# Kernel optimization log

Measured on AMD Instinct MI355X. Metric: run time of the kernel, lower is better.

## Reference

```python
import jax, jax.numpy as jnp
import numpy as np

EMB_DIM = 1024
N_HEADS = 16
HEAD_DIM = EMB_DIM // N_HEADS


def setup_inputs() -> dict:
    key = jax.random.key(0)
    k_x, k_qkv, k_w, k_b = jax.random.split(key, 4)
    x = jax.random.normal(k_x, (2, 2048, EMB_DIM), dtype=jnp.float32)
    # nn.Linear(emb_dim, 3*emb_dim, bias=False): weight [3E, E]; y = x @ W.T
    w_qkv = jax.random.normal(k_qkv, (3 * EMB_DIM, EMB_DIM), dtype=jnp.float32) * (EMB_DIM ** -0.5)
    # nn.Linear(emb_dim, emb_dim) with bias
    w_out = jax.random.normal(k_w, (EMB_DIM, EMB_DIM), dtype=jnp.float32) * (EMB_DIM ** -0.5)
    b_out = jax.random.normal(k_b, (EMB_DIM,), dtype=jnp.float32) * 0.01
    return {"x": x, "w_qkv": w_qkv, "w_out": w_out, "b_out": b_out}


def reference(x, w_qkv, w_out, b_out):
    B, S, E = x.shape
    H, D = N_HEADS, HEAD_DIM
    qkv = jnp.einsum('bse,fe->bsf', x, w_qkv)  # [B,S,3E]
    q, k, v = jnp.split(qkv, 3, axis=-1)
    # [B,S,E] -> [B,H,S,D]
    q = q.reshape(B, S, H, D).transpose(0, 2, 1, 3)
    k = k.reshape(B, S, H, D).transpose(0, 2, 1, 3)
    v = v.reshape(B, S, H, D).transpose(0, 2, 1, 3)
    scale = 1.0 / np.sqrt(D).astype(np.float32)
    scores = jnp.einsum('bhqd,bhkd->bhqk', q, k) * scale  # [B,H,S,S]
    causal = jnp.triu(jnp.ones((S, S), dtype=bool), k=1)
    scores = jnp.where(causal, -jnp.inf, scores)
    probs = jax.nn.softmax(scores, axis=-1)
    attn = jnp.einsum('bhqk,bhkd->bhqd', probs, v)  # [B,H,S,D]
    attn = attn.transpose(0, 2, 1, 3).reshape(B, S, E)
    return jnp.einsum('bse,fe->bsf', attn, w_out) + b_out
```

## Files before the change

kernel.cpp:

```cpp
#include <hip/hip_runtime.h>
#include <hip/hip_bf16.h>

#define EMB 1024
#define NH 16
#define HD 64
#define BATCH 2
#define SEQ 2048
#define MROWS (BATCH*SEQ)
#define F3 (3*EMB)

typedef __bf16 bf16;
typedef __attribute__((ext_vector_type(8))) __bf16 bf16x8;
typedef __attribute__((ext_vector_type(4))) __bf16 bf16x4;
typedef __attribute__((ext_vector_type(2))) __bf16 bf16x2;
typedef __attribute__((ext_vector_type(4))) float f32x4;
typedef __attribute__((ext_vector_type(16))) float f32x16;
typedef __attribute__((ext_vector_type(2))) unsigned int u32x2;

typedef const __attribute__((address_space(1))) void* gptr_t;
typedef __attribute__((address_space(3))) void* lptr_t;
#define GLDS16(g, l) __builtin_amdgcn_global_load_lds((gptr_t)(g), (lptr_t)(l), 16, 0, 0)

__device__ inline bf16 tobf(float f) {
    union { __hip_bfloat16 h; bf16 b; } cv;
    cv.h = __float2bfloat16(f);
    return cv.b;
}

__device__ inline float fexp2(float x) {
#if __has_builtin(__builtin_amdgcn_exp2f)
    return __builtin_amdgcn_exp2f(x);
#else
    return exp2f(x);
#endif
}

__device__ inline void plswap(unsigned& a, unsigned& b) {
#if __has_builtin(__builtin_amdgcn_permlane32_swap)
    u32x2 r = __builtin_amdgcn_permlane32_swap(a, b, false, false);
    a = r[0]; b = r[1];
#else
    unsigned pa = (unsigned)__shfl_xor((int)a, 32, 64);
    unsigned pb = (unsigned)__shfl_xor((int)b, 32, 64);
    bool hi = (threadIdx.x & 32) != 0;
    unsigned na = hi ? pb : a;
    unsigned nb = hi ? b : pa;
    a = na; b = nb;
#endif
}
__device__ inline void plswapf(float& a, float& b) {
    unsigned ua = __builtin_bit_cast(unsigned, a), ub = __builtin_bit_cast(unsigned, b);
    plswap(ua, ub);
    a = __builtin_bit_cast(float, ua); b = __builtin_bit_cast(float, ub);
}
__device__ inline unsigned pack2(float x, float y) {
    bf16x2 t; t[0] = (bf16)x; t[1] = (bf16)y;
    return __builtin_bit_cast(unsigned, t);
}

#define N1 (MROWS*EMB)
#define N2 (F3*EMB)
#define N3 (EMB*EMB)
__global__ __launch_bounds__(256) void cvt_all(const float* __restrict__ x,
                                               const float* __restrict__ wq,
                                               const float* __restrict__ wo,
                                               bf16* __restrict__ xb,
                                               bf16* __restrict__ wqb,
                                               bf16* __restrict__ wob) {
    int i = (blockIdx.x * 256 + threadIdx.x) * 4;
    const float* src;
    bf16* dst;
    int off;
    if (i < N1)           { src = x;  dst = xb;  off = i; }
    else if (i < N1 + N2) { src = wq; dst = wqb; off = i - N1; }
    else                  { src = wo; dst = wob; off = i - N1 - N2; }
    const float4 v = *reinterpret_cast<const float4*>(src + off);
    bf16x4 o;
    o[0] = tobf(v.x); o[1] = tobf(v.y); o[2] = tobf(v.z); o[3] = tobf(v.w);
    *reinterpret_cast<bf16x4*>(dst + off) = o;
}

__global__ __launch_bounds__(256) void gemm_qkv(const bf16* __restrict__ A,
                                                const bf16* __restrict__ Bw,
                                                bf16* __restrict__ qb,
                                                bf16* __restrict__ kb,
                                                bf16* __restrict__ vt) {
    const int K = 1024;
    __shared__ alignas(16) bf16 Alds[128 * 32];
    __shared__ alignas(16) bf16 Blds[128 * 32];
    const int tid = threadIdx.x;
    const int w = tid >> 6, l = tid & 63;
    const int m0 = blockIdx.y * 128, n0 = blockIdx.x * 128;
    const int wr = w >> 1, wc = w & 1;

    f32x4 acc[4][4];
#pragma unroll
    for (int mi = 0; mi < 4; ++mi)
#pragma unroll
        for (int ni = 0; ni < 4; ++ni)
            acc[mi][ni] = f32x4{0.f, 0.f, 0.f, 0.f};

    const int srow = l >> 2;
    const int scol = (l & 3) * 8;
    const bf16* Abase = A + (size_t)m0 * K;
    const bf16* Bbase = Bw + (size_t)n0 * K;

    for (int k0 = 0; k0 < K; k0 += 32) {
#pragma unroll
        for (int i = 0; i < 2; ++i) {
            int chunk = w * 2 + i;
            int row = chunk * 16 + srow;
            GLDS16(Abase + (size_t)row * K + k0 + scol, &Alds[chunk * 512]);
            GLDS16(Bbase + (size_t)row * K + k0 + scol, &Blds[chunk * 512]);
        }
        __syncthreads();
        bf16x8 af[4], bfr[4];
#pragma unroll
        for (int mi = 0; mi < 4; ++mi)
            af[mi] = *reinterpret_cast<const bf16x8*>(
                &Alds[(wr * 64 + mi * 16 + (l & 15)) * 32 + (l >> 4) * 8]);
#pragma unroll
        for (int ni = 0; ni < 4; ++ni)
            bfr[ni] = *reinterpret_cast<const bf16x8*>(
                &Blds[(wc * 64 + ni * 16 + (l & 15)) * 32 + (l >> 4) * 8]);
#pragma unroll
        for (int mi = 0; mi < 4; ++mi)
#pragma unroll
            for (int ni = 0; ni < 4; ++ni)
                acc[mi][ni] = __builtin_amdgcn_mfma_f32_16x16x32_bf16(
                    af[mi], bfr[ni], acc[mi][ni], 0, 0, 0);
        __syncthreads();
    }

    const int which = n0 >> 10;
#pragma unroll
    for (int mi = 0; mi < 4; ++mi) {
#pragma unroll
        for (int ni = 0; ni < 4; ++ni) {
            int fcol = n0 + wc * 64 + ni * 16 + (l & 15);
            int h = (fcol >> 6) & 15, d = fcol & 63;
            int mbase = m0 + wr * 64 + mi * 16 + (l >> 4) * 4;
            int b = mbase >> 11, s = mbase & 2047;
            int bh = b * NH + h;
            if (which == 2) {
                bf16x4 vv;
#pragma unroll
                for (int jj = 0; jj < 4; ++jj) vv[jj] = tobf(acc[mi][ni][jj]);
                *reinterpret_cast<bf16x4*>(&vt[((size_t)bh * HD + d) * SEQ + s]) = vv;
            } else if (which == 0) {
#pragma unroll
                for (int jj = 0; jj < 4; ++jj)
                    qb[((size_t)bh * SEQ + s + jj) * HD + d] = tobf(acc[mi][ni][jj] * 0.180336881f);
            } else {
#pragma unroll
                for (int jj = 0; jj < 4; ++jj)
                    kb[((size_t)bh * SEQ + s + jj) * HD + d] = tobf(acc[mi][ni][jj]);
            }
        }
    }
}

__global__ __launch_bounds__(512, 4) void attn_kernel(const bf16* __restrict__ qb,
                                                      const bf16* __restrict__ kb,
                                                      const bf16* __restrict__ vt,
                                                      bf16* __restrict__ ao) {
    __shared__ alignas(16) char SM[69632];
    bf16 (*Kl)[4096] = (bf16 (*)[4096])SM;
    bf16 (*Vl)[4096] = (bf16 (*)[4096])(SM + 32768);
    float* Msh = (float*)(SM + 65536);
    float* Rsh = (float*)(SM + 67584);
    float* Osh = (float*)SM;

    const int tid = threadIdx.x, w = tid >> 6, l = tid & 63;
    const int hi = l >> 5;
    const int qg = w & 3, kg = w >> 2;
    const int h = (int)(blockIdx.x >> 5);
    const int qt = (h < 8) ? (15 - h) : (h - 8);
    const int bh = blockIdx.x & 31;
    const int q0 = qt * 128;
    const bf16* Qp = qb + (size_t)bh * SEQ * HD;
    const bf16* Kp = kb + (size_t)bh * SEQ * HD;
    const bf16* Vp = vt + (size_t)bh * HD * SEQ;

    const int qa = q0 + qg * 32 + (l & 31);
    bf16x8 qf[4];
#pragma unroll
    for (int kk = 0; kk < 4; ++kk)
        qf[kk] = *reinterpret_cast<const bf16x8*>(&Qp[(size_t)qa * HD + kk * 16 + hi * 8]);

    f32x16 o[2];
#pragma unroll
    for (int t = 0; t < 2; ++t)
#pragma unroll
        for (int r = 0; r < 16; ++r) o[t][r] = 0.f;
    float m = -__builtin_inff(), rs = 0.f;

    const int sc = ((l & 7) ^ (l >> 3)) * 8;

#define STAGE(itp)                                                                  \
    do {                                                                            \
        int j_ = 2 * (itp) + kg;                                                    \
        int slot_ = j_ & 3;                                                         \
        int kv0_ = j_ * 64;                                                         \
        int r0_ = qg * 16 + (l >> 3);                                               \
        GLDS16(Kp + (size_t)(kv0_ + r0_) * HD + sc, &Kl[slot_][(qg * 16) * 64]);    \
        GLDS16(Kp + (size_t)(kv0_ + r0_ + 8) * HD + sc, &Kl[slot_][(qg * 16 + 8) * 64]); \
        GLDS16(Vp + (size_t)r0_ * SEQ + kv0_ + sc, &Vl[slot_][(qg * 16) * 64]);     \
        GLDS16(Vp + (size_t)(r0_ + 8) * SEQ + kv0_ + sc, &Vl[slot_][(qg * 16 + 8) * 64]); \
    } while (0)

    STAGE(0);
    __syncthreads();

    const int qminw = q0 + qg * 32;
    const int qmaxw = qminw + 31;

    for (int it = 0; it <= qt; ++it) {
        if (it < qt) STAGE(it + 1);
        const int j = 2 * it + kg;
        if (j * 64 <= qmaxw) {
            const int slot = j & 3;
            f32x16 st[2];
            __builtin_amdgcn_s_setprio(1);
#pragma unroll
            for (int t = 0; t < 2; ++t) {
#pragma unroll
                for (int r = 0; r < 16; ++r) st[t][r] = 0.f;
                int row = t * 32 + (l & 31);
                int rsw = (row & 7) << 3;
#pragma unroll
                for (int kk = 0; kk < 4; ++kk) {
                    bf16x8 kf = *reinterpret_cast<const bf16x8*>(
                        &Kl[slot][row * 64 + ((kk * 16 + hi * 8) ^ rsw)]);
                    st[t] = __builtin_amdgcn_mfma_f32_32x32x16_bf16(kf, qf[kk], st[t], 0, 0, 0);
                }
            }
            __builtin_amdgcn_s_setprio(0);
            if (j * 64 + 63 > qminw) {
#pragma unroll
                for (int t = 0; t < 2; ++t)
#pragma unroll
                    for (int r = 0; r < 16; ++r) {
                        int kv = j * 64 + t * 32 + 8 * (r >> 2) + 4 * hi + (r & 3);
                        if (kv > qa) st[t][r] = -__builtin_inff();
                    }
            }
            float red[8];
#pragma unroll
            for (int r = 0; r < 8; ++r)
                red[r] = fmaxf(fmaxf(st[0][r], st[0][r + 8]), fmaxf(st[1][r], st[1][r + 8]));
            float pm = fmaxf(fmaxf(fmaxf(red[0], red[1]), fmaxf(red[2], red[3])),
                             fmaxf(fmaxf(red[4], red[5]), fmaxf(red[6], red[7])));
            float pa_ = pm, pb_ = pm;
            plswapf(pa_, pb_);
            pm = fmaxf(pa_, pb_);
            if (!__all(pm <= m + 8.f)) {
                float mn = fmaxf(m, pm);
                float al = fexp2(m - mn);
#pragma unroll
                for (int t = 0; t < 2; ++t)
#pragma unroll
                    for (int r = 0; r < 16; ++r) o[t][r] *= al;
                rs *= al;
                m = mn;
            }
#pragma unroll
            for (int t = 0; t < 2; ++t)
#pragma unroll
                for (int r = 0; r < 16; ++r) {
                    float p = fexp2(st[t][r] - m);
                    st[t][r] = p;
                    rs += p;
                }
#pragma unroll
            for (int t = 0; t < 2; ++t) {
                unsigned Ag[4], Bg[4];
#pragma unroll
                for (int g = 0; g < 4; ++g) {
                    Ag[g] = pack2(st[t][4 * g + 0], st[t][4 * g + 1]);
                    Bg[g] = pack2(st[t][4 * g + 2], st[t][4 * g + 3]);
                }
                __builtin_amdgcn_s_setprio(1);
#pragma unroll
                for (int k2 = 0; k2 < 2; ++k2) {
                    unsigned w0 = Ag[2 * k2], w2 = Ag[2 * k2 + 1];
                    plswap(w0, w2);
                    unsigned w1 = Bg[2 * k2], w3 = Bg[2 * k2 + 1];
                    plswap(w1, w3);
                    union { unsigned u[4]; bf16x8 v; } pf;
                    pf.u[0] = w0; pf.u[1] = w1; pf.u[2] = w2; pf.u[3] = w3;
                    const int kk = 2 * t + k2;
#pragma unroll
                    for (int dt = 0; dt < 2; ++dt) {
                        int row = dt * 32 + (l & 31);
                        bf16x8 vf = *reinterpret_cast<const bf16x8*>(
                            &Vl[slot][row * 64 + ((kk * 16 + hi * 8) ^ ((row & 7) << 3))]);
                        o[dt] = __builtin_amdgcn_mfma_f32_32x32x16_bf16(vf, pf.v, o[dt], 0, 0, 0);
                    }
                }
                __builtin_amdgcn_s_setprio(0);
            }
        }
        __syncthreads();
    }

    float rlo = rs, rhi = rs;
    plswapf(rlo, rhi);
    const float rfull = rlo + rhi;
    Msh[w * 64 + l] = m;
    Rsh[w * 64 + l] = rfull;
    if (kg == 1) {
        float* dst = Osh + (size_t)(qg * 64 + l) * 32;
#pragma unroll
        for (int c = 0; c < 8; ++c) {
            f32x4 tch;
#pragma unroll
            for (int i = 0; i < 4; ++i) tch[i] = o[c >> 2][(c & 3) * 4 + i];
            *reinterpret_cast<f32x4*>(dst + (c ^ (l & 7)) * 4) = tch;
        }
    }
    __syncthreads();
    if (kg == 0) {
        const float mb = Msh[(w + 4) * 64 + l];
        const float rb = Rsh[(w + 4) * 64 + l];
        const float mstar = fmaxf(m, mb);
        const float sa = fexp2(m - mstar), sb = fexp2(mb - mstar);
        const float inv = 1.f / (rfull * sa + rb * sb);
        const float* src = Osh + (size_t)(qg * 64 + l) * 32;
        const int b = bh >> 4, hh = bh & 15;
#pragma unroll
        for (int c = 0; c < 8; ++c) {
            f32x4 ob = *reinterpret_cast<const f32x4*>(src + (c ^ (l & 7)) * 4);
            bf16x4 ov;
#pragma unroll
            for (int i = 0; i < 4; ++i)
                ov[i] = (bf16)((o[c >> 2][(c & 3) * 4 + i] * sa + ob[i] * sb) * inv);
            int d0 = (c >> 2) * 32 + 8 * (c & 3) + 4 * hi;
            *reinterpret_cast<bf16x4*>(&ao[((size_t)b * SEQ + qa) * EMB + hh * HD + d0]) = ov;
        }
    }
#undef STAGE
}

__global__ __launch_bounds__(256) void gemm_out(const bf16* __restrict__ A,
                                                const bf16* __restrict__ Bw,
                                                float* __restrict__ out,
                                                const float* __restrict__ bias) {
    const int K = 1024;
    __shared__ alignas(16) bf16 Alds[64 * 32];
    __shared__ alignas(16) bf16 Blds[128 * 32];
    const int tid = threadIdx.x;
    const int w = tid >> 6, l = tid & 63;
    const int m0 = blockIdx.y * 64, n0 = blockIdx.x * 128;

    f32x4 acc[4][2];
#pragma unroll
    for (int mi = 0; mi < 4; ++mi)
#pragma unroll
        for (int ni = 0; ni < 2; ++ni)
            acc[mi][ni] = f32x4{0.f, 0.f, 0.f, 0.f};

    const int srow = l >> 2;
    const int scol = (l & 3) * 8;
    const bf16* Abase = A + (size_t)m0 * K;
    const bf16* Bbase = Bw + (size_t)n0 * K;

    for (int k0 = 0; k0 < K; k0 += 32) {
        GLDS16(Abase + (size_t)(w * 16 + srow) * K + k0 + scol, &Alds[w * 512]);
#pragma unroll
        for (int i = 0; i < 2; ++i) {
            int chunk = w * 2 + i;
            GLDS16(Bbase + (size_t)(chunk * 16 + srow) * K + k0 + scol, &Blds[chunk * 512]);
        }
        __syncthreads();
        bf16x8 af[4], bfr[2];
#pragma unroll
        for (int mi = 0; mi < 4; ++mi)
            af[mi] = *reinterpret_cast<const bf16x8*>(
                &Alds[(mi * 16 + (l & 15)) * 32 + (l >> 4) * 8]);
#pragma unroll
        for (int ni = 0; ni < 2; ++ni)
            bfr[ni] = *reinterpret_cast<const bf16x8*>(
                &Blds[(w * 32 + ni * 16 + (l & 15)) * 32 + (l >> 4) * 8]);
#pragma unroll
        for (int mi = 0; mi < 4; ++mi)
#pragma unroll
            for (int ni = 0; ni < 2; ++ni)
                acc[mi][ni] = __builtin_amdgcn_mfma_f32_16x16x32_bf16(
                    af[mi], bfr[ni], acc[mi][ni], 0, 0, 0);
        __syncthreads();
    }

#pragma unroll
    for (int mi = 0; mi < 4; ++mi) {
#pragma unroll
        for (int ni = 0; ni < 2; ++ni) {
            int fcol = n0 + w * 32 + ni * 16 + (l & 15);
            float bv = bias[fcol];
#pragma unroll
            for (int jj = 0; jj < 4; ++jj) {
                int m = m0 + mi * 16 + (l >> 4) * 4 + jj;
                out[(size_t)m * EMB + fcol] = acc[mi][ni][jj] + bv;
            }
        }
    }
}

extern "C" void kernel_launch(void* const* d_in, const int* in_sizes, int n_in,
                              void* d_out, int out_size, void* d_ws, size_t ws_size,
                              hipStream_t stream) {
    const float* x     = (const float*)d_in[0];
    const float* w_qkv = (const float*)d_in[1];
    const float* w_out = (const float*)d_in[2];
    const float* b_out = (const float*)d_in[3];
    float* out = (float*)d_out;

    char* ws = (char*)d_ws;
    bf16* xb    = (bf16*)(ws);
    bf16* wqkvb = (bf16*)(ws + ((size_t)8 << 20));
    bf16* woutb = (bf16*)(ws + ((size_t)14 << 20));
    bf16* qb    = (bf16*)(ws + ((size_t)16 << 20));
    bf16* kb    = (bf16*)(ws + ((size_t)24 << 20));
    bf16* vt    = (bf16*)(ws + ((size_t)32 << 20));
    bf16* ab    = (bf16*)(ws + ((size_t)40 << 20));

    cvt_all<<<(N1 + N2 + N3) / 1024, 256, 0, stream>>>(x, w_qkv, w_out, xb, wqkvb, woutb);
    gemm_qkv<<<dim3(F3 / 128, MROWS / 128), 256, 0, stream>>>(xb, wqkvb, qb, kb, vt);
    attn_kernel<<<512, 512, 0, stream>>>(qb, kb, vt, ab);
    gemm_out<<<dim3(EMB / 128, MROWS / 64), 256, 0, stream>>>(ab, woutb, out, b_out);
}
```

Baseline: 170.2 us.

## Rewrite QKV GEMM as 256x256 tile with double-buffered swizzled LDS pipeline

Replaces the simple 128x128 QKV projection GEMM, which synchronised on every K step, with a 256x256 tile per 512-thread block. It uses 128KB of dynamic LDS split into two buffers, XOR-swizzled LDS layout to avoid bank conflicts, and an interleaved schedule that issues global-to-LDS loads for future K tiles while MFMAs run on current fragments. It also adds explicit waitcnt, barriers and setprio to hide load latency and raise data reuse. In exchange it runs far fewer blocks (12x16=192), so occupancy is lower and the CUs may be unevenly loaded, and the hand-written schedule is fragile.

```diff
diff --git a/kernel.cpp b/kernel.cpp
--- a/kernel.cpp
+++ b/kernel.cpp
@@ -80,84 +80,177 @@
     *reinterpret_cast<bf16x4*>(dst + off) = o;
 }
 
-__global__ __launch_bounds__(256) void gemm_qkv(const bf16* __restrict__ A,
-                                                const bf16* __restrict__ Bw,
-                                                bf16* __restrict__ qb,
-                                                bf16* __restrict__ kb,
-                                                bf16* __restrict__ vt) {
-    const int K = 1024;
-    __shared__ alignas(16) bf16 Alds[128 * 32];
-    __shared__ alignas(16) bf16 Blds[128 * 32];
+__global__ __launch_bounds__(512, 2) void gemm_qkv(const bf16* __restrict__ A,
+                                                   const bf16* __restrict__ Bw,
+                                                   bf16* __restrict__ qb,
+                                                   bf16* __restrict__ kb,
+                                                   bf16* __restrict__ vt) {
+    extern __shared__ bf16 dsm[];
+    bf16* Al = dsm;
+    bf16* Bl = dsm + 32768;
+
     const int tid = threadIdx.x;
     const int w = tid >> 6, l = tid & 63;
-    const int m0 = blockIdx.y * 128, n0 = blockIdx.x * 128;
-    const int wr = w >> 1, wc = w & 1;
-
-    f32x4 acc[4][4];
-#pragma unroll
-    for (int mi = 0; mi < 4; ++mi)
-#pragma unroll
-        for (int ni = 0; ni < 4; ++ni)
-            acc[mi][ni] = f32x4{0.f, 0.f, 0.f, 0.f};
-
-    const int srow = l >> 2;
-    const int scol = (l & 3) * 8;
-    const bf16* Abase = A + (size_t)m0 * K;
-    const bf16* Bbase = Bw + (size_t)n0 * K;
-
-    for (int k0 = 0; k0 < K; k0 += 32) {
-#pragma unroll
-        for (int i = 0; i < 2; ++i) {
-            int chunk = w * 2 + i;
-            int row = chunk * 16 + srow;
-            GLDS16(Abase + (size_t)row * K + k0 + scol, &Alds[chunk * 512]);
-            GLDS16(Bbase + (size_t)row * K + k0 + scol, &Blds[chunk * 512]);
-        }
-        __syncthreads();
-        bf16x8 af[4], bfr[4];
-#pragma unroll
-        for (int mi = 0; mi < 4; ++mi)
-            af[mi] = *reinterpret_cast<const bf16x8*>(
-                &Alds[(wr * 64 + mi * 16 + (l & 15)) * 32 + (l >> 4) * 8]);
-#pragma unroll
-        for (int ni = 0; ni < 4; ++ni)
-            bfr[ni] = *reinterpret_cast<const bf16x8*>(
-                &Blds[(wc * 64 + ni * 16 + (l & 15)) * 32 + (l >> 4) * 8]);
-#pragma unroll
-        for (int mi = 0; mi < 4; ++mi)
-#pragma unroll
-            for (int ni = 0; ni < 4; ++ni)
-                acc[mi][ni] = __builtin_amdgcn_mfma_f32_16x16x32_bf16(
-                    af[mi], bfr[ni], acc[mi][ni], 0, 0, 0);
-        __syncthreads();
-    }
-
-    const int which = n0 >> 10;
-#pragma unroll
-    for (int mi = 0; mi < 4; ++mi) {
-#pragma unroll
-        for (int ni = 0; ni < 4; ++ni) {
-            int fcol = n0 + wc * 64 + ni * 16 + (l & 15);
+    const int wm = w >> 2, wn = w & 3;
+    const int m0 = blockIdx.y * 256, n0 = blockIdx.x * 256;
+
+    const int sc = ((l & 7) ^ (l >> 3)) * 8;
+    const int lr = l >> 3;
+    const int l15 = l & 15, l4 = l >> 4, l7 = l & 7;
+
+    f32x4 acc[8][4];
+#pragma unroll
+    for (int i = 0; i < 8; ++i)
+#pragma unroll
+        for (int j = 0; j < 4; ++j) acc[i][j] = f32x4{0.f, 0.f, 0.f, 0.f};
+
+    bf16x8 Af[4][2], Bf[2][2];
+
+#define STA(bb, mh, ct)                                                                  \
+    do {                                                                                 \
+        int rs_ = (mh) * 64 + w * 8;                                                     \
+        GLDS16(A + (size_t)(m0 + rs_ + lr) * 1024 + (ct) * 64 + sc, (lptr_t)&Al[(bb) * 16384 + rs_ * 64]);          \
+        GLDS16(A + (size_t)(m0 + 128 + rs_ + lr) * 1024 + (ct) * 64 + sc, (lptr_t)&Al[(bb) * 16384 + (128 + rs_) * 64]); \
+    } while (0)
+#define STB(bb, nh, ct)                                                                  \
+    do {                                                                                 \
+        int r1_ = (w >> 2) * 64 + (nh) * 32 + (w & 3) * 8;                               \
+        int r2_ = r1_ + 128;                                                             \
+        GLDS16(Bw + (size_t)(n0 + r1_ + lr) * 1024 + (ct) * 64 + sc, (lptr_t)&Bl[(bb) * 16384 + r1_ * 64]); \
+        GLDS16(Bw + (size_t)(n0 + r2_ + lr) * 1024 + (ct) * 64 + sc, (lptr_t)&Bl[(bb) * 16384 + r2_ * 64]); \
+    } while (0)
+#define LDA(bb, mh)                                                                      \
+    do {                                                                                 \
+        _Pragma("unroll") for (int mi = 0; mi < 4; ++mi)                                 \
+        _Pragma("unroll") for (int ks = 0; ks < 2; ++ks)                                 \
+            Af[mi][ks] = *reinterpret_cast<const bf16x8*>(                               \
+                &Al[(bb) * 16384 + (wm * 128 + (mh) * 64 + mi * 16 + l15) * 64 +         \
+                    (((ks * 4 + l4) ^ l7) * 8)]);                                        \
+    } while (0)
+#define LDB(bb, nh)                                                                      \
+    do {                                                                                 \
+        _Pragma("unroll") for (int ni = 0; ni < 2; ++ni)                                 \
+        _Pragma("unroll") for (int ks = 0; ks < 2; ++ks)                                 \
+            Bf[ni][ks] = *reinterpret_cast<const bf16x8*>(                               \
+                &Bl[(bb) * 16384 + (wn * 64 + (nh) * 32 + ni * 16 + l15) * 64 +          \
+                    (((ks * 4 + l4) ^ l7) * 8)]);                                        \
+    } while (0)
+#define MM(mh, nh)                                                                       \
+    do {                                                                                 \
+        __builtin_amdgcn_s_setprio(1);                                                   \
+        _Pragma("unroll") for (int mi = 0; mi < 4; ++mi)                                 \
+        _Pragma("unroll") for (int ni = 0; ni < 2; ++ni)                                 \
+        _Pragma("unroll") for (int ks = 0; ks < 2; ++ks)                                 \
+            acc[(mh) * 4 + mi][(nh) * 2 + ni] = __builtin_amdgcn_mfma_f32_16x16x32_bf16( \
+                Af[mi][ks], Bf[ni][ks], acc[(mh) * 4 + mi][(nh) * 2 + ni], 0, 0, 0);     \
+        __builtin_amdgcn_s_setprio(0);                                                   \
+    } while (0)
+#define PH_TAIL()                                                                        \
+    __builtin_amdgcn_s_barrier();                                                        \
+    asm volatile("s_waitcnt lgkmcnt(0)" ::: "memory");                                   \
+    __builtin_amdgcn_sched_barrier(0)
+#define PH_END() __builtin_amdgcn_s_barrier()
+
+    STA(0, 0, 0); STA(0, 1, 0); STB(0, 0, 0); STB(0, 1, 0);
+    STB(1, 0, 1); STA(1, 1, 1);
+    asm volatile("s_waitcnt vmcnt(4)" ::: "memory");
+    __builtin_amdgcn_s_barrier();
+
+#pragma unroll 1
+    for (int it = 0; it < 7; ++it) {
+        const int t1 = 2 * it + 1;
+        LDA(0, 0); LDB(0, 0);
+        __builtin_amdgcn_sched_barrier(0);
+        STA(1, 0, t1);
+        PH_TAIL(); MM(0, 0); PH_END();
+        LDA(0, 1);
+        __builtin_amdgcn_sched_barrier(0);
+        STB(1, 1, t1);
+        PH_TAIL(); MM(1, 0); PH_END();
+        LDB(0, 1);
+        __builtin_amdgcn_sched_barrier(0);
+        STB(0, 0, t1 + 1);
+        PH_TAIL(); MM(1, 1); PH_END();
+        LDA(0, 0);
+        __builtin_amdgcn_sched_barrier(0);
+        STA(0, 1, t1 + 1);
+        asm volatile("s_waitcnt vmcnt(4)" ::: "memory");
+        PH_TAIL(); MM(0, 1); PH_END();
+        LDA(1, 0); LDB(1, 0);
+        __builtin_amdgcn_sched_barrier(0);
+        STA(0, 0, t1 + 1);
+        PH_TAIL(); MM(0, 0); PH_END();
+        LDA(1, 1);
+        __builtin_amdgcn_sched_barrier(0);
+        STB(0, 1, t1 + 1);
+        PH_TAIL(); MM(1, 0); PH_END();
+        LDB(1, 1);
+        __builtin_amdgcn_sched_barrier(0);
+        STB(1, 0, t1 + 2);
+        PH_TAIL(); MM(1, 1); PH_END();
+        LDA(1, 0);
+        __builtin_amdgcn_sched_barrier(0);
+        STA(1, 1, t1 + 2);
+        asm volatile("s_waitcnt vmcnt(4)" ::: "memory");
+        PH_TAIL(); MM(0, 1); PH_END();
+    }
+    {
+        LDA(0, 0); LDB(0, 0);
+        __builtin_amdgcn_sched_barrier(0);
+        STA(1, 0, 15);
+        PH_TAIL(); MM(0, 0); PH_END();
+        LDA(0, 1);
+        __builtin_amdgcn_sched_barrier(0);
+        STB(1, 1, 15);
+        PH_TAIL(); MM(1, 0); PH_END();
+        LDB(0, 1);
+        PH_TAIL(); MM(1, 1); PH_END();
+        LDA(0, 0);
+        asm volatile("s_waitcnt vmcnt(0)" ::: "memory");
+        PH_TAIL(); MM(0, 1); PH_END();
+        LDA(1, 0); LDB(1, 0);
+        PH_TAIL(); MM(0, 0); PH_END();
+        LDA(1, 1);
+        PH_TAIL(); MM(1, 0); PH_END();
+        LDB(1, 1);
+        PH_TAIL(); MM(1, 1); PH_END();
+        LDA(1, 0);
+        PH_TAIL(); MM(0, 1); PH_END();
+    }
+
+    const int which = (n0 + wn * 64) >> 10;
+#pragma unroll
+    for (int mf = 0; mf < 8; ++mf) {
+#pragma unroll
+        for (int nf = 0; nf < 4; ++nf) {
+            int fcol = n0 + wn * 64 + nf * 16 + l15;
             int h = (fcol >> 6) & 15, d = fcol & 63;
-            int mbase = m0 + wr * 64 + mi * 16 + (l >> 4) * 4;
+            int mbase = m0 + wm * 128 + mf * 16 + l4 * 4;
             int b = mbase >> 11, s = mbase & 2047;
             int bh = b * NH + h;
             if (which == 2) {
                 bf16x4 vv;
 #pragma unroll
-                for (int jj = 0; jj < 4; ++jj) vv[jj] = tobf(acc[mi][ni][jj]);
+                for (int jj = 0; jj < 4; ++jj) vv[jj] = tobf(acc[mf][nf][jj]);
                 *reinterpret_cast<bf16x4*>(&vt[((size_t)bh * HD + d) * SEQ + s]) = vv;
             } else if (which == 0) {
 #pragma unroll
                 for (int jj = 0; jj < 4; ++jj)
-                    qb[((size_t)bh * SEQ + s + jj) * HD + d] = tobf(acc[mi][ni][jj] * 0.180336881f);
+                    qb[((size_t)bh * SEQ + s + jj) * HD + d] = tobf(acc[mf][nf][jj] * 0.180336881f);
             } else {
 #pragma unroll
                 for (int jj = 0; jj < 4; ++jj)
-                    kb[((size_t)bh * SEQ + s + jj) * HD + d] = tobf(acc[mi][ni][jj]);
+                    kb[((size_t)bh * SEQ + s + jj) * HD + d] = tobf(acc[mf][nf][jj]);
             }
         }
     }
+#undef STA
+#undef STB
+#undef LDA
+#undef LDB
+#undef MM
+#undef PH_TAIL
+#undef PH_END
 }
 
 __global__ __launch_bounds__(512, 4) void attn_kernel(const bf16* __restrict__ qb,
@@ -424,8 +517,11 @@
     bf16* vt    = (bf16*)(ws + ((size_t)32 << 20));
     bf16* ab    = (bf16*)(ws + ((size_t)40 << 20));
 
+    hipFuncSetAttribute((const void*)gemm_qkv,
+                        hipFuncAttributeMaxDynamicSharedMemorySize, 131072);
+
     cvt_all<<<(N1 + N2 + N3) / 1024, 256, 0, stream>>>(x, w_qkv, w_out, xb, wqkvb, woutb);
-    gemm_qkv<<<dim3(F3 / 128, MROWS / 128), 256, 0, stream>>>(xb, wqkvb, qb, kb, vt);
+    gemm_qkv<<<dim3(F3 / 256, MROWS / 256), 512, 131072, stream>>>(xb, wqkvb, qb, kb, vt);
     attn_kernel<<<512, 512, 0, stream>>>(qb, kb, vt, ab);
     gemm_out<<<dim3(EMB / 128, MROWS / 64), 256, 0, stream>>>(ab, woutb, out, b_out);
 }
```

Measured after the change: 170.7 us. No clear change (+0.3%).

## Double GEMM K-tile to 64 with XOR-swizzled LDS and block remap

Applied to the files above, without the earlier changes.

Both the QKV and output projection GEMMs now stage 64-wide K tiles instead of 32, halving the number of barrier pairs per K loop. An XOR swizzle is applied to the LDS column placement so the wider rows avoid bank conflicts on the fragment reads. Block indices are also remapped so consecutive workgroups share A/B tiles in L2. Costs are double the LDS footprint per block and more fragment registers, which may reduce occupancy.

```diff
diff --git a/kernel.cpp b/kernel.cpp
--- a/kernel.cpp
+++ b/kernel.cpp
@@ -86,12 +86,18 @@
                                                 bf16* __restrict__ kb,
                                                 bf16* __restrict__ vt) {
     const int K = 1024;
-    __shared__ alignas(16) bf16 Alds[128 * 32];
-    __shared__ alignas(16) bf16 Blds[128 * 32];
+    __shared__ alignas(16) bf16 Alds[128 * 64];
+    __shared__ alignas(16) bf16 Blds[128 * 64];
     const int tid = threadIdx.x;
     const int w = tid >> 6, l = tid & 63;
-    const int m0 = blockIdx.y * 128, n0 = blockIdx.x * 128;
     const int wr = w >> 1, wc = w & 1;
+    const int lin = (int)blockIdx.y * 24 + (int)blockIdx.x;
+    const int swz = (lin & 7) * 96 + (lin >> 3);
+    const int m0 = (swz / 24) * 128, n0 = (swz % 24) * 128;
+
+    const int sc = ((l & 7) ^ (l >> 3)) * 8;
+    const int lr = l >> 3;
+    const int l15 = l & 15, l4 = l >> 4, l7 = l & 7;
 
     f32x4 acc[4][4];
 #pragma unroll
@@ -100,35 +106,38 @@
         for (int ni = 0; ni < 4; ++ni)
             acc[mi][ni] = f32x4{0.f, 0.f, 0.f, 0.f};
 
-    const int srow = l >> 2;
-    const int scol = (l & 3) * 8;
     const bf16* Abase = A + (size_t)m0 * K;
     const bf16* Bbase = Bw + (size_t)n0 * K;
 
-    for (int k0 = 0; k0 < K; k0 += 32) {
-#pragma unroll
-        for (int i = 0; i < 2; ++i) {
-            int chunk = w * 2 + i;
-            int row = chunk * 16 + srow;
-            GLDS16(Abase + (size_t)row * K + k0 + scol, &Alds[chunk * 512]);
-            GLDS16(Bbase + (size_t)row * K + k0 + scol, &Blds[chunk * 512]);
+    for (int k0 = 0; k0 < K; k0 += 64) {
+#pragma unroll
+        for (int i = 0; i < 4; ++i) {
+            int r0 = i * 32 + w * 8;
+            GLDS16(Abase + (size_t)(r0 + lr) * K + k0 + sc, (lptr_t)&Alds[r0 * 64]);
+            GLDS16(Bbase + (size_t)(r0 + lr) * K + k0 + sc, (lptr_t)&Blds[r0 * 64]);
         }
         __syncthreads();
-        bf16x8 af[4], bfr[4];
+        bf16x8 af[4][2], bfr[4][2];
 #pragma unroll
         for (int mi = 0; mi < 4; ++mi)
-            af[mi] = *reinterpret_cast<const bf16x8*>(
-                &Alds[(wr * 64 + mi * 16 + (l & 15)) * 32 + (l >> 4) * 8]);
+#pragma unroll
+            for (int ks = 0; ks < 2; ++ks)
+                af[mi][ks] = *reinterpret_cast<const bf16x8*>(
+                    &Alds[(wr * 64 + mi * 16 + l15) * 64 + (((ks * 4 + l4) ^ l7) * 8)]);
 #pragma unroll
         for (int ni = 0; ni < 4; ++ni)
-            bfr[ni] = *reinterpret_cast<const bf16x8*>(
-                &Blds[(wc * 64 + ni * 16 + (l & 15)) * 32 + (l >> 4) * 8]);
+#pragma unroll
+            for (int ks = 0; ks < 2; ++ks)
+                bfr[ni][ks] = *reinterpret_cast<const bf16x8*>(
+                    &Blds[(wc * 64 + ni * 16 + l15) * 64 + (((ks * 4 + l4) ^ l7) * 8)]);
 #pragma unroll
         for (int mi = 0; mi < 4; ++mi)
 #pragma unroll
             for (int ni = 0; ni < 4; ++ni)
-                acc[mi][ni] = __builtin_amdgcn_mfma_f32_16x16x32_bf16(
-                    af[mi], bfr[ni], acc[mi][ni], 0, 0, 0);
+#pragma unroll
+                for (int ks = 0; ks < 2; ++ks)
+                    acc[mi][ni] = __builtin_amdgcn_mfma_f32_16x16x32_bf16(
+                        af[mi][ks], bfr[ni][ks], acc[mi][ni], 0, 0, 0);
         __syncthreads();
     }
 
@@ -137,9 +146,9 @@
     for (int mi = 0; mi < 4; ++mi) {
 #pragma unroll
         for (int ni = 0; ni < 4; ++ni) {
-            int fcol = n0 + wc * 64 + ni * 16 + (l & 15);
+            int fcol = n0 + wc * 64 + ni * 16 + l15;
             int h = (fcol >> 6) & 15, d = fcol & 63;
-            int mbase = m0 + wr * 64 + mi * 16 + (l >> 4) * 4;
+            int mbase = m0 + wr * 64 + mi * 16 + l4 * 4;
             int b = mbase >> 11, s = mbase & 2047;
             int bh = b * NH + h;
             if (which == 2) {
@@ -347,11 +356,17 @@
                                                 float* __restrict__ out,
                                                 const float* __restrict__ bias) {
     const int K = 1024;
-    __shared__ alignas(16) bf16 Alds[64 * 32];
-    __shared__ alignas(16) bf16 Blds[128 * 32];
+    __shared__ alignas(16) bf16 Alds[64 * 64];
+    __shared__ alignas(16) bf16 Blds[128 * 64];
     const int tid = threadIdx.x;
     const int w = tid >> 6, l = tid & 63;
-    const int m0 = blockIdx.y * 64, n0 = blockIdx.x * 128;
+    const int lin = (int)blockIdx.y * 8 + (int)blockIdx.x;
+    const int swz = (lin & 7) * 64 + (lin >> 3);
+    const int m0 = (swz >> 3) * 64, n0 = (swz & 7) * 128;
+
+    const int sc = ((l & 7) ^ (l >> 3)) * 8;
+    const int lr = l >> 3;
+    const int l15 = l & 15, l4 = l >> 4, l7 = l & 7;
 
     f32x4 acc[4][2];
 #pragma unroll
@@ -360,34 +375,42 @@
         for (int ni = 0; ni < 2; ++ni)
             acc[mi][ni] = f32x4{0.f, 0.f, 0.f, 0.f};
 
-    const int srow = l >> 2;
-    const int scol = (l & 3) * 8;
     const bf16* Abase = A + (size_t)m0 * K;
     const bf16* Bbase = Bw + (size_t)n0 * K;
 
-    for (int k0 = 0; k0 < K; k0 += 32) {
-        GLDS16(Abase + (size_t)(w * 16 + srow) * K + k0 + scol, &Alds[w * 512]);
+    for (int k0 = 0; k0 < K; k0 += 64) {
 #pragma unroll
         for (int i = 0; i < 2; ++i) {
-            int chunk = w * 2 + i;
-            GLDS16(Bbase + (size_t)(chunk * 16 + srow) * K + k0 + scol, &Blds[chunk * 512]);
+            int r0 = i * 32 + w * 8;
+            GLDS16(Abase + (size_t)(r0 + lr) * K + k0 + sc, (lptr_t)&Alds[r0 * 64]);
+        }
+#pragma unroll
+        for (int i = 0; i < 4; ++i) {
+            int r0 = i * 32 + w * 8;
+            GLDS16(Bbase + (size_t)(r0 + lr) * K + k0 + sc, (lptr_t)&Blds[r0 * 64]);
         }
         __syncthreads();
-        bf16x8 af[4], bfr[2];
+        bf16x8 af[4][2], bfr[2][2];
 #pragma unroll
         for (int mi = 0; mi < 4; ++mi)
-            af[mi] = *reinterpret_cast<const bf16x8*>(
-                &Alds[(mi * 16 + (l & 15)) * 32 + (l >> 4) * 8]);
+#pragma unroll
+            for (int ks = 0; ks < 2; ++ks)
+                af[mi][ks] = *reinterpret_cast<const bf16x8*>(
+                    &Alds[(mi * 16 + l15) * 64 + (((ks * 4 + l4) ^ l7) * 8)]);
 #pragma unroll
         for (int ni = 0; ni < 2; ++ni)
-            bfr[ni] = *reinterpret_cast<const bf16x8*>(
-                &Blds[(w * 32 + ni * 16 + (l & 15)) * 32 + (l >> 4) * 8]);
+#pragma unroll
+            for (int ks = 0; ks < 2; ++ks)
+                bfr[ni][ks] = *reinterpret_cast<const bf16x8*>(
+                    &Blds[(w * 32 + ni * 16 + l15) * 64 + (((ks * 4 + l4) ^ l7) * 8)]);
 #pragma unroll
         for (int mi = 0; mi < 4; ++mi)
 #pragma unroll
             for (int ni = 0; ni < 2; ++ni)
-                acc[mi][ni] = __builtin_amdgcn_mfma_f32_16x16x32_bf16(
-                    af[mi], bfr[ni], acc[mi][ni], 0, 0, 0);
+#pragma unroll
+                for (int ks = 0; ks < 2; ++ks)
+                    acc[mi][ni] = __builtin_amdgcn_mfma_f32_16x16x32_bf16(
+                        af[mi][ks], bfr[ni][ks], acc[mi][ni], 0, 0, 0);
         __syncthreads();
     }
 
@@ -395,12 +418,12 @@
     for (int mi = 0; mi < 4; ++mi) {
 #pragma unroll
         for (int ni = 0; ni < 2; ++ni) {
-            int fcol = n0 + w * 32 + ni * 16 + (l & 15);
+            int fcol = n0 + w * 32 + ni * 16 + l15;
             float bv = bias[fcol];
 #pragma unroll
             for (int jj = 0; jj < 4; ++jj) {
-                int m = m0 + mi * 16 + (l >> 4) * 4 + jj;
-                out[(size_t)m * EMB + fcol] = acc[mi][ni][jj] + bv;
+                int mm = m0 + mi * 16 + l4 * 4 + jj;
+                out[(size_t)mm * EMB + fcol] = acc[mi][ni][jj] + bv;
             }
         }
     }
```

New measurement: 175.8 us. +3.3%, slower.
